# Optimization experiments

Hardware: AMD Instinct MI355X
Metric: run time of the kernel (lower is better)

## Reference

```python
import jax, jax.numpy as jnp
import numpy as np

N_NODES = 50000


def _sage_conv(x, src, dst, Wl, bl, Wr):
    # mean aggregation of neighbor (source) features at destination nodes
    msg = x[src]                                              # [E, d]
    agg = jax.ops.segment_sum(msg, dst, num_segments=N_NODES)  # [N, d]
    cnt = jax.ops.segment_sum(jnp.ones((src.shape[0],), x.dtype), dst,
                              num_segments=N_NODES)            # [N]
    agg = agg / jnp.clip(cnt, 1.0)[:, None]
    # lin_l(aggregated) + lin_r(self), bias only on lin_l (PyG default)
    return agg @ Wl + bl + x @ Wr


def setup_inputs() -> dict:
    key = jax.random.key(0)
    ks = jax.random.split(key, 8)
    d = 128
    E = 800000
    x = jax.random.normal(ks[0], (N_NODES, d), dtype=jnp.float32)
    edge_index = jax.random.randint(ks[1], (2, E), 0, N_NODES, dtype=jnp.int64)
    s1 = 1.0 / np.sqrt(d)
    s2 = 1.0 / np.sqrt(32)
    return {
        "x": x,
        "edge_index": edge_index,
        "W1l": jax.random.normal(ks[2], (d, 32), jnp.float32) * s1,
        "b1": jnp.zeros((32,), jnp.float32),
        "W1r": jax.random.normal(ks[3], (d, 32), jnp.float32) * s1,
        "W2l": jax.random.normal(ks[4], (32, 32), jnp.float32) * s2,
        "b2": jnp.zeros((32,), jnp.float32),
        "W2r": jax.random.normal(ks[5], (32, 32), jnp.float32) * s2,
    }


def reference(x, edge_index, W1l, b1, W1r, W2l, b2, W2r):
    src, dst = edge_index[0], edge_index[1]
    h = jax.nn.relu(_sage_conv(x, src, dst, W1l, b1, W1r))
    return _sage_conv(h, src, dst, W2l, b2, W2r)
```

## Files before the change

kernel.cpp:

```cpp
#include <hip/hip_runtime.h>
#include <hip/hip_bf16.h>


#define N_NODES 50000
#define NB 196
#define GB 256

__global__ __launch_bounds__(256) void kproj(
    const float* __restrict__ in, const float* __restrict__ Wl,
    const float* __restrict__ Wr, float* __restrict__ z, int N, int K) {
  __shared__ float xs[64 * 68];
  __shared__ float ws[64 * 64];
  const int t = threadIdx.x;
  const int n0 = blockIdx.x * 64;
  const int nvalid = (N - n0) < 64 ? (N - n0) : 64;

  const int tx = t & 15, ty = t >> 4;
  const int c0 = tx * 4;
  const int nl = ty * 4;

  float acc[4][4];
#pragma unroll
  for (int i = 0; i < 4; i++)
#pragma unroll
    for (int j = 0; j < 4; j++) acc[i][j] = 0.f;

  for (int kc = 0; kc < K; kc += 64) {
    const int KC = (K - kc) < 64 ? (K - kc) : 64;
    for (int i = t; i < KC * 32; i += 256) {
      int k = i >> 5, c = i & 31;
      ws[k * 64 + c] = Wl[(size_t)(kc + k) * 32 + c];
      ws[k * 64 + 32 + c] = Wr[(size_t)(kc + k) * 32 + c];
    }
    {
      const int kq = KC >> 2;
      const int sh = (KC == 64) ? 4 : 3;
      const int lim = nvalid * kq;
      for (int i = t; i < lim; i += 256) {
        int n = i >> sh, q = i & (kq - 1);
        float4 v = *(const float4*)(in + (size_t)(n0 + n) * K + kc + q * 4);
        *(float4*)(xs + n * 68 + q * 4) = v;
      }
    }
    __syncthreads();

    const float* x0 = xs + (nl + 0) * 68;
    const float* x1 = xs + (nl + 1) * 68;
    const float* x2 = xs + (nl + 2) * 68;
    const float* x3 = xs + (nl + 3) * 68;
    for (int k = 0; k < KC; k += 4) {
      float4 xa = *(const float4*)(x0 + k);
      float4 xb = *(const float4*)(x1 + k);
      float4 xc = *(const float4*)(x2 + k);
      float4 xd = *(const float4*)(x3 + k);
#pragma unroll
      for (int kk = 0; kk < 4; kk++) {
        float4 w = *(const float4*)(ws + (k + kk) * 64 + c0);
        float va = ((const float*)&xa)[kk];
        float vb = ((const float*)&xb)[kk];
        float vc = ((const float*)&xc)[kk];
        float vd = ((const float*)&xd)[kk];
        acc[0][0] += va * w.x; acc[0][1] += va * w.y;
        acc[0][2] += va * w.z; acc[0][3] += va * w.w;
        acc[1][0] += vb * w.x; acc[1][1] += vb * w.y;
        acc[1][2] += vb * w.z; acc[1][3] += vb * w.w;
        acc[2][0] += vc * w.x; acc[2][1] += vc * w.y;
        acc[2][2] += vc * w.z; acc[2][3] += vc * w.w;
        acc[3][0] += vd * w.x; acc[3][1] += vd * w.y;
        acc[3][2] += vd * w.z; acc[3][3] += vd * w.w;
      }
    }
    __syncthreads();
  }
#pragma unroll
  for (int i = 0; i < 4; i++) {
    int node = n0 + nl + i;
    if (node < N) {
      float4 v = make_float4(acc[i][0], acc[i][1], acc[i][2], acc[i][3]);
      *(float4*)(z + (size_t)node * 64 + c0) = v;
    }
  }
}

__global__ __launch_bounds__(256) void k_bcount(const int* __restrict__ dst,
                                                int* __restrict__ blkhist,
                                                int E, int chunk) {
  __shared__ int h[NB];
  const int t = threadIdx.x, b = blockIdx.x;
  if (t < NB) h[t] = 0;
  __syncthreads();
  const int e0 = b * chunk;
  int e1 = e0 + chunk;
  if (e1 > E) e1 = E;
  for (int e = e0 + t; e < e1; e += 256) atomicAdd(&h[dst[e] >> 8], 1);
  __syncthreads();
  if (t < NB) blkhist[b * NB + t] = h[t];
}

__global__ __launch_bounds__(256) void k_bscan(int* __restrict__ blkhist,
                                               int* __restrict__ bb, int E) {
  __shared__ int sc[256];
  const int t = threadIdx.x;
  int run = 0;
  if (t < NB) {
    for (int b = 0; b < GB; b += 8) {
      int v[8];
#pragma unroll
      for (int i = 0; i < 8; i++) v[i] = blkhist[(b + i) * NB + t];
#pragma unroll
      for (int i = 0; i < 8; i++) {
        blkhist[(b + i) * NB + t] = run;
        run += v[i];
      }
    }
  }
  sc[t] = (t < NB) ? run : 0;
  __syncthreads();
  for (int off = 1; off < 256; off <<= 1) {
    int tmp = (t >= off) ? sc[t - off] : 0;
    __syncthreads();
    sc[t] += tmp;
    __syncthreads();
  }
  if (t < NB) bb[t] = sc[t] - run;
  if (t == 0) bb[NB] = E;
}

__global__ __launch_bounds__(256) void k_bscatter(
    const int* __restrict__ src, const int* __restrict__ dst,
    const int* __restrict__ blkhist, const int* __restrict__ bb,
    int* __restrict__ ebuf, int E, int chunk) {
  __shared__ int cur[NB];
  const int t = threadIdx.x, b = blockIdx.x;
  if (t < NB) cur[t] = bb[t] + blkhist[b * NB + t];
  __syncthreads();
  const int e0 = b * chunk;
  int e1 = e0 + chunk;
  if (e1 > E) e1 = E;
  for (int e = e0 + t; e < e1; e += 256) {
    int d = dst[e], s = src[e];
    int pos = atomicAdd(&cur[d >> 8], 1);
    ebuf[pos] = (s << 8) | (d & 255);
  }
}

__global__ __launch_bounds__(256) void k_bsort(const int* __restrict__ ebuf,
                                               const int* __restrict__ bb,
                                               int* __restrict__ adj,
                                               int* __restrict__ row_ptr,
                                               int N, int E) {
  __shared__ int cnt[256];
  __shared__ int sc[256];
  const int t = threadIdx.x, k = blockIdx.x;
  const int r0 = bb[k], r1 = bb[k + 1];
  cnt[t] = 0;
  __syncthreads();
  for (int i = r0 + t; i < r1; i += 256) atomicAdd(&cnt[ebuf[i] & 255], 1);
  __syncthreads();
  sc[t] = cnt[t];
  __syncthreads();
  for (int off = 1; off < 256; off <<= 1) {
    int tmp = (t >= off) ? sc[t - off] : 0;
    __syncthreads();
    sc[t] += tmp;
    __syncthreads();
  }
  const int excl = sc[t] - cnt[t];
  const int node = (k << 8) + t;
  if (node < N) row_ptr[node] = r0 + excl;
  if (k == 0 && t == 0) row_ptr[N] = E;
  __syncthreads();
  cnt[t] = r0 + excl;
  __syncthreads();
  for (int i = r0 + t; i < r1; i += 256) {
    int v = ebuf[i];
    int pos = atomicAdd(&cnt[v & 255], 1);
    adj[pos] = v >> 8;
  }
}

__global__ __launch_bounds__(256) void k_agg(
    const float* __restrict__ zc, const int* __restrict__ adj,
    const int* __restrict__ row_ptr, const float* __restrict__ bias,
    float* __restrict__ out, int N, int do_relu) {
  const int t = threadIdx.x;
  const int j = t & 31;
  const int node = blockIdx.x * 8 + (t >> 5);
  if (node >= N) return;
  const int r0 = row_ptr[node], r1 = row_ptr[node + 1];
  float a0 = 0.f, a1 = 0.f, a2 = 0.f, a3 = 0.f;
  int e = r0;
  for (; e + 4 <= r1; e += 4) {
    int s0 = adj[e], s1 = adj[e + 1], s2 = adj[e + 2], s3 = adj[e + 3];
    a0 += zc[(size_t)s0 * 64 + j];
    a1 += zc[(size_t)s1 * 64 + j];
    a2 += zc[(size_t)s2 * 64 + j];
    a3 += zc[(size_t)s3 * 64 + j];
  }
  for (; e < r1; ++e) a0 += zc[(size_t)adj[e] * 64 + j];
  float sum = (a0 + a1) + (a2 + a3);
  const int deg = r1 - r0;
  float m = sum / (float)(deg > 1 ? deg : 1);
  float v = m + bias[j] + zc[(size_t)node * 64 + 32 + j];
  out[(size_t)node * 32 + j] = do_relu ? fmaxf(v, 0.f) : v;
}

extern "C" void kernel_launch(void* const* d_in, const int* in_sizes, int n_in,
                              void* d_out, int out_size, void* d_ws,
                              size_t ws_size, hipStream_t stream) {
  const float* x = (const float*)d_in[0];
  const int* ei = (const int*)d_in[1];
  const float* W1l = (const float*)d_in[2];
  const float* b1 = (const float*)d_in[3];
  const float* W1r = (const float*)d_in[4];
  const float* W2l = (const float*)d_in[5];
  const float* b2 = (const float*)d_in[6];
  const float* W2r = (const float*)d_in[7];
  float* out = (float*)d_out;

  const int N = N_NODES;
  const int E = in_sizes[1] / 2;

  float* zc = (float*)d_ws;
  int* ebuf = (int*)(zc + (size_t)N * 64);
  int* adj = ebuf + E;
  int* row_ptr = adj + E;
  int* bb = row_ptr + N + 1;
  int* blkhist = bb + NB + 1;
  float* h = out;

  const int* srcp = ei;
  const int* dstp = ei + E;

  const int chunk = (E + GB - 1) / GB;
  const int nblk_proj = (N + 63) / 64;
  const int nblk_agg = (N + 7) / 8;

  k_bcount<<<GB, 256, 0, stream>>>(dstp, blkhist, E, chunk);
  k_bscan<<<1, 256, 0, stream>>>(blkhist, bb, E);
  k_bscatter<<<GB, 256, 0, stream>>>(srcp, dstp, blkhist, bb, ebuf, E, chunk);
  k_bsort<<<NB, 256, 0, stream>>>(ebuf, bb, adj, row_ptr, N, E);

  kproj<<<nblk_proj, 256, 0, stream>>>(x, W1l, W1r, zc, N, 128);
  k_agg<<<nblk_agg, 256, 0, stream>>>(zc, adj, row_ptr, b1, h, N, 1);
  kproj<<<nblk_proj, 256, 0, stream>>>(h, W2l, W2r, zc, N, 32);
  k_agg<<<nblk_agg, 256, 0, stream>>>(zc, adj, row_ptr, b2, out, N, 0);
}
```

Before: 188.8 us.

## Replace CSR build with bucket-local LDS atomic aggregation and fuse layer-2 projection

```diff
diff --git a/kernel.cpp b/kernel.cpp
--- a/kernel.cpp
+++ b/kernel.cpp
@@ -1,5 +1,4 @@
 #include <hip/hip_runtime.h>
-#include <hip/hip_bf16.h>
 
 
 #define N_NODES 50000
@@ -144,65 +143,129 @@
   }
 }
 
-__global__ __launch_bounds__(256) void k_bsort(const int* __restrict__ ebuf,
-                                               const int* __restrict__ bb,
-                                               int* __restrict__ adj,
-                                               int* __restrict__ row_ptr,
-                                               int N, int E) {
+__global__ __launch_bounds__(1024) void k_fagg1(
+    const float* __restrict__ zc, const int* __restrict__ ebuf,
+    const int* __restrict__ bb, const float* __restrict__ b1,
+    const float* __restrict__ W2l, const float* __restrict__ W2r,
+    float* __restrict__ z2, int N) {
+  __shared__ float acc[256 * 32];
+  __shared__ float w2p[32 * 64];
   __shared__ int cnt[256];
-  __shared__ int sc[256];
-  const int t = threadIdx.x, k = blockIdx.x;
+  __shared__ float bsh[32];
+  const int t = threadIdx.x;
+  const int k = blockIdx.x;
+  for (int i = t; i < 256 * 32; i += 1024) acc[i] = 0.f;
+  if (t < 256) cnt[t] = 0;
+  for (int i = t; i < 2048; i += 1024) {
+    int j = i >> 6, c = i & 63;
+    w2p[i] = (c < 32) ? W2l[j * 32 + c] : W2r[j * 32 + (c - 32)];
+  }
+  if (t < 32) bsh[t] = b1[t];
+  __syncthreads();
+
   const int r0 = bb[k], r1 = bb[k + 1];
-  cnt[t] = 0;
-  __syncthreads();
-  for (int i = r0 + t; i < r1; i += 256) atomicAdd(&cnt[ebuf[i] & 255], 1);
-  __syncthreads();
-  sc[t] = cnt[t];
-  __syncthreads();
-  for (int off = 1; off < 256; off <<= 1) {
-    int tmp = (t >= off) ? sc[t - off] : 0;
-    __syncthreads();
-    sc[t] += tmp;
-    __syncthreads();
-  }
-  const int excl = sc[t] - cnt[t];
-  const int node = (k << 8) + t;
-  if (node < N) row_ptr[node] = r0 + excl;
-  if (k == 0 && t == 0) row_ptr[N] = E;
-  __syncthreads();
-  cnt[t] = r0 + excl;
-  __syncthreads();
-  for (int i = r0 + t; i < r1; i += 256) {
-    int v = ebuf[i];
-    int pos = atomicAdd(&cnt[v & 255], 1);
-    adj[pos] = v >> 8;
-  }
-}
-
-__global__ __launch_bounds__(256) void k_agg(
-    const float* __restrict__ zc, const int* __restrict__ adj,
-    const int* __restrict__ row_ptr, const float* __restrict__ bias,
-    float* __restrict__ out, int N, int do_relu) {
+  const int gid = t >> 5, j = t & 31;
+  int e = r0 + gid;
+  for (; e + 96 < r1; e += 128) {
+    int v0 = ebuf[e], v1 = ebuf[e + 32], v2 = ebuf[e + 64], v3 = ebuf[e + 96];
+    float f0 = zc[(size_t)(v0 >> 8) * 64 + j];
+    float f1 = zc[(size_t)(v1 >> 8) * 64 + j];
+    float f2 = zc[(size_t)(v2 >> 8) * 64 + j];
+    float f3 = zc[(size_t)(v3 >> 8) * 64 + j];
+    atomicAdd(&acc[(v0 & 255) * 32 + j], f0);
+    atomicAdd(&acc[(v1 & 255) * 32 + j], f1);
+    atomicAdd(&acc[(v2 & 255) * 32 + j], f2);
+    atomicAdd(&acc[(v3 & 255) * 32 + j], f3);
+    if (j == 0) {
+      atomicAdd(&cnt[v0 & 255], 1);
+      atomicAdd(&cnt[v1 & 255], 1);
+      atomicAdd(&cnt[v2 & 255], 1);
+      atomicAdd(&cnt[v3 & 255], 1);
+    }
+  }
+  for (; e < r1; e += 32) {
+    int v = ebuf[e];
+    float f = zc[(size_t)(v >> 8) * 64 + j];
+    atomicAdd(&acc[(v & 255) * 32 + j], f);
+    if (j == 0) atomicAdd(&cnt[v & 255], 1);
+  }
+  __syncthreads();
+
+  const int n0 = k << 8;
+#pragma unroll
+  for (int i = 0; i < 8; i++) {
+    const int nl = gid * 8 + i;
+    const int node = n0 + nl;
+    if (node >= N) break;
+    const int dg = cnt[nl];
+    float h = acc[nl * 32 + j] / (float)(dg > 1 ? dg : 1) + bsh[j] +
+              zc[(size_t)node * 64 + 32 + j];
+    h = fmaxf(h, 0.f);
+    float a0 = 0.f, a1 = 0.f;
+#pragma unroll
+    for (int jj = 0; jj < 32; jj++) {
+      float hj = __shfl(h, jj, 32);
+      a0 += hj * w2p[jj * 64 + j];
+      a1 += hj * w2p[jj * 64 + 32 + j];
+    }
+    z2[(size_t)node * 64 + j] = a0;
+    z2[(size_t)node * 64 + 32 + j] = a1;
+  }
+}
+
+__global__ __launch_bounds__(1024) void k_fagg2(
+    const float* __restrict__ z2, const int* __restrict__ ebuf,
+    const int* __restrict__ bb, const float* __restrict__ b2,
+    float* __restrict__ out, int N) {
+  __shared__ float acc[256 * 32];
+  __shared__ int cnt[256];
+  __shared__ float bsh[32];
   const int t = threadIdx.x;
-  const int j = t & 31;
-  const int node = blockIdx.x * 8 + (t >> 5);
-  if (node >= N) return;
-  const int r0 = row_ptr[node], r1 = row_ptr[node + 1];
-  float a0 = 0.f, a1 = 0.f, a2 = 0.f, a3 = 0.f;
-  int e = r0;
-  for (; e + 4 <= r1; e += 4) {
-    int s0 = adj[e], s1 = adj[e + 1], s2 = adj[e + 2], s3 = adj[e + 3];
-    a0 += zc[(size_t)s0 * 64 + j];
-    a1 += zc[(size_t)s1 * 64 + j];
-    a2 += zc[(size_t)s2 * 64 + j];
-    a3 += zc[(size_t)s3 * 64 + j];
-  }
-  for (; e < r1; ++e) a0 += zc[(size_t)adj[e] * 64 + j];
-  float sum = (a0 + a1) + (a2 + a3);
-  const int deg = r1 - r0;
-  float m = sum / (float)(deg > 1 ? deg : 1);
-  float v = m + bias[j] + zc[(size_t)node * 64 + 32 + j];
-  out[(size_t)node * 32 + j] = do_relu ? fmaxf(v, 0.f) : v;
+  const int k = blockIdx.x;
+  for (int i = t; i < 256 * 32; i += 1024) acc[i] = 0.f;
+  if (t < 256) cnt[t] = 0;
+  if (t < 32) bsh[t] = b2[t];
+  __syncthreads();
+
+  const int r0 = bb[k], r1 = bb[k + 1];
+  const int gid = t >> 5, j = t & 31;
+  int e = r0 + gid;
+  for (; e + 96 < r1; e += 128) {
+    int v0 = ebuf[e], v1 = ebuf[e + 32], v2 = ebuf[e + 64], v3 = ebuf[e + 96];
+    float f0 = z2[(size_t)(v0 >> 8) * 64 + j];
+    float f1 = z2[(size_t)(v1 >> 8) * 64 + j];
+    float f2 = z2[(size_t)(v2 >> 8) * 64 + j];
+    float f3 = z2[(size_t)(v3 >> 8) * 64 + j];
+    atomicAdd(&acc[(v0 & 255) * 32 + j], f0);
+    atomicAdd(&acc[(v1 & 255) * 32 + j], f1);
+    atomicAdd(&acc[(v2 & 255) * 32 + j], f2);
+    atomicAdd(&acc[(v3 & 255) * 32 + j], f3);
+    if (j == 0) {
+      atomicAdd(&cnt[v0 & 255], 1);
+      atomicAdd(&cnt[v1 & 255], 1);
+      atomicAdd(&cnt[v2 & 255], 1);
+      atomicAdd(&cnt[v3 & 255], 1);
+    }
+  }
+  for (; e < r1; e += 32) {
+    int v = ebuf[e];
+    float f = z2[(size_t)(v >> 8) * 64 + j];
+    atomicAdd(&acc[(v & 255) * 32 + j], f);
+    if (j == 0) atomicAdd(&cnt[v & 255], 1);
+  }
+  __syncthreads();
+
+  const int n0 = k << 8;
+#pragma unroll
+  for (int i = 0; i < 8; i++) {
+    const int nl = gid * 8 + i;
+    const int node = n0 + nl;
+    if (node >= N) break;
+    const int dg = cnt[nl];
+    float v = acc[nl * 32 + j] / (float)(dg > 1 ? dg : 1) + bsh[j] +
+              z2[(size_t)node * 64 + 32 + j];
+    out[(size_t)node * 32 + j] = v;
+  }
 }
 
 extern "C" void kernel_launch(void* const* d_in, const int* in_sizes, int n_in,
@@ -222,27 +285,21 @@
   const int E = in_sizes[1] / 2;
 
   float* zc = (float*)d_ws;
-  int* ebuf = (int*)(zc + (size_t)N * 64);
-  int* adj = ebuf + E;
-  int* row_ptr = adj + E;
-  int* bb = row_ptr + N + 1;
+  float* zc2 = zc + (size_t)N * 64;
+  int* ebuf = (int*)(zc2 + (size_t)N * 64);
+  int* bb = ebuf + E;
   int* blkhist = bb + NB + 1;
-  float* h = out;
 
   const int* srcp = ei;
   const int* dstp = ei + E;
 
   const int chunk = (E + GB - 1) / GB;
   const int nblk_proj = (N + 63) / 64;
-  const int nblk_agg = (N + 7) / 8;
 
   k_bcount<<<GB, 256, 0, stream>>>(dstp, blkhist, E, chunk);
   k_bscan<<<1, 256, 0, stream>>>(blkhist, bb, E);
   k_bscatter<<<GB, 256, 0, stream>>>(srcp, dstp, blkhist, bb, ebuf, E, chunk);
-  k_bsort<<<NB, 256, 0, stream>>>(ebuf, bb, adj, row_ptr, N, E);
-
   kproj<<<nblk_proj, 256, 0, stream>>>(x, W1l, W1r, zc, N, 128);
-  k_agg<<<nblk_agg, 256, 0, stream>>>(zc, adj, row_ptr, b1, h, N, 1);
-  kproj<<<nblk_proj, 256, 0, stream>>>(h, W2l, W2r, zc, N, 32);
-  k_agg<<<nblk_agg, 256, 0, stream>>>(zc, adj, row_ptr, b2, out, N, 0);
-}
+  k_fagg1<<<NB, 1024, 0, stream>>>(zc, ebuf, bb, b1, W2l, W2r, zc2, N);
+  k_fagg2<<<NB, 1024, 0, stream>>>(zc2, ebuf, bb, b2, out, N);
+}
```

Result: slower. 497.9 us (+163.8%).
